# Kernel tuning notes

Hardware: AMD Instinct MI355X
Metric: run time of the kernel (lower is better)

## Reference

```python
import jax, jax.numpy as jnp
import numpy as np

N = 50000      # nodes
E = 800000     # edges (before self-loops)
F_IN = 256     # nfeat
HEADS = 8      # nhead
C1 = 16        # hidden_sizes (per-head channels of conv1)
NCLS = 40      # nclass
NEG_SLOPE = 0.2


def setup_inputs() -> dict:
    key = jax.random.key(0)
    ks = jax.random.split(key, 12)
    s = 0.1
    x = jax.random.normal(ks[0], (N, F_IN), dtype=jnp.float32)
    edge_index = jax.random.randint(ks[1], (2, E), 0, N, dtype=jnp.int64)
    edge_attr = jax.random.normal(ks[2], (E,), dtype=jnp.float32)  # unused by forward
    W1 = jax.random.normal(ks[3], (F_IN, HEADS * C1), dtype=jnp.float32) * s
    att_src1 = jax.random.normal(ks[4], (HEADS, C1), dtype=jnp.float32) * s
    att_dst1 = jax.random.normal(ks[5], (HEADS, C1), dtype=jnp.float32) * s
    b1 = jnp.zeros((HEADS * C1,), dtype=jnp.float32)
    W2 = jax.random.normal(ks[6], (HEADS * C1, NCLS), dtype=jnp.float32) * s
    att_src2 = jax.random.normal(ks[7], (1, NCLS), dtype=jnp.float32) * s
    att_dst2 = jax.random.normal(ks[8], (1, NCLS), dtype=jnp.float32) * s
    b2 = jnp.zeros((NCLS,), dtype=jnp.float32)
    return {"x": x, "edge_index": edge_index, "edge_attr": edge_attr,
            "W1": W1, "att_src1": att_src1, "att_dst1": att_dst1, "b1": b1,
            "W2": W2, "att_src2": att_src2, "att_dst2": att_dst2, "b2": b2}


def gat_layer(x, W, att_src, att_dst, bias, src, dst, concat):
    """PyG-style GATConv (eval mode, no dropout). src/dst include self-loops."""
    H, C = att_src.shape
    h = (x @ W).reshape(-1, H, C)                     # [N,H,C]
    a_src = (h * att_src[None]).sum(-1)               # [N,H]
    a_dst = (h * att_dst[None]).sum(-1)               # [N,H]
    e = jax.nn.leaky_relu(a_src[src] + a_dst[dst], NEG_SLOPE)  # [Etot,H]
    # segment softmax over destination neighborhoods
    m = jax.ops.segment_max(e, dst, num_segments=N)   # [N,H]
    m = jax.lax.stop_gradient(jnp.where(jnp.isfinite(m), m, 0.0))
    p = jnp.exp(e - m[dst])
    denom = jax.ops.segment_sum(p, dst, num_segments=N)
    alpha = p / (denom[dst] + 1e-16)                  # [Etot,H]
    out = jax.ops.segment_sum(alpha[:, :, None] * h[src], dst, num_segments=N)  # [N,H,C]
    out = out.reshape(-1, H * C) if concat else out.mean(axis=1)
    return out + bias


def reference(x, edge_index, edge_attr, W1, att_src1, att_dst1, b1, W2, att_src2, att_dst2, b2):
    # add self loops (PyG GATConv default)
    loops = jnp.arange(N, dtype=edge_index.dtype)
    src = jnp.concatenate([edge_index[0], loops])
    dst = jnp.concatenate([edge_index[1], loops])
    # eval mode: F.dropout is identity
    h = jax.nn.elu(gat_layer(x, W1, att_src1, att_dst1, b1, src, dst, concat=True))
    final = gat_layer(h, W2, att_src2, att_dst2, b2, src, dst, concat=False)
    return final, jax.nn.log_softmax(final, axis=1)
```

## Files before the change

### kernel.cpp

```cpp
#include <hip/hip_runtime.h>

#define NN 50000
#define EE 800000
#define FIN 256
#define HD 8
#define C1 16
#define HC 128
#define NC 40
#define NEG 0.2f
#define CAP 64
#define R2 32
#define BM 64
#define NB_P 98
#define GB1 (NB_P * 8)
#define NP_N (NN / 8)

typedef __attribute__((ext_vector_type(8))) short short8;
typedef __attribute__((ext_vector_type(4))) float f32x4;
union FragU { uint4 u; short8 s; };

__device__ __forceinline__ float leaky(float v){ return v > 0.f ? v : NEG * v; }

__device__ __forceinline__ unsigned int f2bf(float f){
  unsigned int u = __float_as_uint(f);
  u += 0x7fffu + ((u >> 16) & 1u);
  return u >> 16;
}
__device__ __forceinline__ unsigned int pack2bf(float a, float b){
  return f2bf(a) | (f2bf(b) << 16);
}
__device__ __forceinline__ float bflo(unsigned int u){ return __uint_as_float(u << 16); }
__device__ __forceinline__ float bfhi(unsigned int u){ return __uint_as_float(u & 0xffff0000u); }

__global__ __launch_bounds__(256) void k_prep(const float* __restrict__ W1,
                                              uint4* __restrict__ W1bfs){
  int f = blockIdx.x * 256 + threadIdx.x;
  int lane = f & 63, nt = (f >> 6) & 7, kt = f >> 9;
  int quad = lane >> 4, l16 = lane & 15;
  const float* src = W1 + (size_t)(kt * 32 + quad * 8) * HC + nt * 16 + l16;
  unsigned int p[4];
#pragma unroll
  for (int jj = 0; jj < 4; jj++){
    float v0 = src[(size_t)(2 * jj) * HC];
    float v1 = src[(size_t)(2 * jj + 1) * HC];
    p[jj] = pack2bf(v0, v1);
  }
  W1bfs[f] = make_uint4(p[0], p[1], p[2], p[3]);
}

__global__ __launch_bounds__(256) void k_gemm1(const float* __restrict__ x,
                                               const uint4* __restrict__ W1bfs,
                                               const float* __restrict__ att_s,
                                               const float* __restrict__ att_d,
                                               const int* __restrict__ ei,
                                               unsigned short* __restrict__ h1b,
                                               float* __restrict__ as1,
                                               float* __restrict__ ad1,
                                               int* __restrict__ cnt,
                                               int* __restrict__ srcp){
  const int tid = threadIdx.x;
  const int part = blockIdx.x & 7, rank = blockIdx.x >> 3;
  const int lo = part * NP_N, hi = lo + NP_N;
  for (int e = rank * 256 + tid; e < EE; e += NB_P * 256){
    int d = ei[EE + e];
    if (d >= lo && d < hi){
      int s = ei[e];
      int pos = atomicAdd(&cnt[d], 1);
      if (pos < CAP) srcp[d * CAP + pos] = s;
    }
  }

  const int wave = tid >> 6, lane = tid & 63;
  const int quad = lane >> 4, l16 = lane & 15;
  const int m0 = blockIdx.x * BM + wave * 16;
  int arow = m0 + l16; if (arow >= NN) arow = NN - 1;
  const float* xr = x + (size_t)arow * FIN;

  f32x4 acc[8];
#pragma unroll
  for (int t = 0; t < 8; t++) acc[t] = (f32x4){0.f, 0.f, 0.f, 0.f};

#pragma unroll
  for (int kt = 0; kt < 8; kt++){
    const float4 a0 = *(const float4*)(xr + kt * 32 + quad * 8);
    const float4 a1 = *(const float4*)(xr + kt * 32 + quad * 8 + 4);
    FragU af;
    af.u = make_uint4(pack2bf(a0.x, a0.y), pack2bf(a0.z, a0.w),
                      pack2bf(a1.x, a1.y), pack2bf(a1.z, a1.w));
    FragU bf[8];
#pragma unroll
    for (int nt = 0; nt < 8; nt++)
      bf[nt].u = W1bfs[(kt * 8 + nt) * 64 + lane];
#pragma unroll
    for (int nt = 0; nt < 8; nt++)
      acc[nt] = __builtin_amdgcn_mfma_f32_16x16x32_bf16(af.s, bf[nt].s, acc[nt], 0, 0, 0);
  }

  float sv[8], dv[8];
#pragma unroll
  for (int h = 0; h < 8; h++){ sv[h] = att_s[h * 16 + l16]; dv[h] = att_d[h * 16 + l16]; }
#pragma unroll
  for (int r = 0; r < 4; r++){
    const int gr = m0 + quad * 4 + r;
    float s[8], d[8];
#pragma unroll
    for (int h = 0; h < 8; h++){ s[h] = acc[h][r] * sv[h]; d[h] = acc[h][r] * dv[h]; }
#pragma unroll
    for (int o = 1; o < 16; o <<= 1){
#pragma unroll
      for (int h = 0; h < 8; h++){ s[h] += __shfl_xor(s[h], o); d[h] += __shfl_xor(d[h], o); }
    }
    if (gr < NN){
#pragma unroll
      for (int h = 0; h < 8; h++)
        h1b[(size_t)gr * HC + h * 16 + l16] = (unsigned short)f2bf(acc[h][r]);
      if (l16 == 0){
        *(float4*)(as1 + gr * 8)     = make_float4(s[0], s[1], s[2], s[3]);
        *(float4*)(as1 + gr * 8 + 4) = make_float4(s[4], s[5], s[6], s[7]);
        *(float4*)(ad1 + gr * 8)     = make_float4(d[0], d[1], d[2], d[3]);
        *(float4*)(ad1 + gr * 8 + 4) = make_float4(d[4], d[5], d[6], d[7]);
      }
    }
  }
}

__global__ __launch_bounds__(64) void k_agg1(const int* __restrict__ srcp,
                                             const int* __restrict__ cnt,
                                             const float* __restrict__ as1,
                                             const float* __restrict__ ad1,
                                             const unsigned short* __restrict__ h1b,
                                             const float* __restrict__ b1,
                                             unsigned short* __restrict__ h2b){
  const int n = blockIdx.x, lane = threadIdx.x;
  const int q = lane >> 4, t = lane & 15, h = t >> 1;
  const int base = n * CAP;
  int deg = cnt[n]; if (deg > CAP) deg = CAP;
  const float adg = ad1[n * 8 + h];
  float m = -3.0e38f, den = 0.f;
  float acc[8];
#pragma unroll
  for (int c = 0; c < 8; c++) acc[c] = 0.f;

  if (q == 0){
    const uint4 hv = *(const uint4*)(h1b + (size_t)n * HC + t * 8);
    m = leaky(as1[n * 8 + h] + adg);
    den = 1.f;
    acc[0] = bflo(hv.x); acc[1] = bfhi(hv.x);
    acc[2] = bflo(hv.y); acc[3] = bfhi(hv.y);
    acc[4] = bflo(hv.z); acc[5] = bfhi(hv.z);
    acc[6] = bflo(hv.w); acc[7] = bfhi(hv.w);
  }

  int i = q;
  int sA = (i < deg) ? srcp[base + i] : n;
  uint4 hA = *(const uint4*)(h1b + (size_t)sA * HC + t * 8);
  float aA = as1[sA * 8 + h];
  int sB = (i + 4 < deg) ? srcp[base + i + 4] : n;
  while (i < deg){
    const uint4 hB = *(const uint4*)(h1b + (size_t)sB * HC + t * 8);
    const float aB = as1[sB * 8 + h];
    const int sC = (i + 8 < deg) ? srcp[base + i + 8] : n;
    float v = leaky(aA + adg);
    float mn = fmaxf(m, v);
    float r = __expf(m - mn), w = __expf(v - mn);
    den = den * r + w;
    acc[0] = acc[0] * r + w * bflo(hA.x); acc[1] = acc[1] * r + w * bfhi(hA.x);
    acc[2] = acc[2] * r + w * bflo(hA.y); acc[3] = acc[3] * r + w * bfhi(hA.y);
    acc[4] = acc[4] * r + w * bflo(hA.z); acc[5] = acc[5] * r + w * bfhi(hA.z);
    acc[6] = acc[6] * r + w * bflo(hA.w); acc[7] = acc[7] * r + w * bfhi(hA.w);
    m = mn;
    hA = hB; aA = aB; sA = sB; sB = sC;
    i += 4;
  }
#pragma unroll
  for (int o = 16; o <= 32; o <<= 1){
    float mo = __shfl_xor(m, o);
    float dno = __shfl_xor(den, o);
    float mn = fmaxf(m, mo);
    float ra = __expf(m - mn), rb = __expf(mo - mn);
    den = den * ra + dno * rb;
#pragma unroll
    for (int c = 0; c < 8; c++){
      float ao = __shfl_xor(acc[c], o);
      acc[c] = acc[c] * ra + ao * rb;
    }
    m = mn;
  }
  if (q == 0){
    float invd = 1.f / (den + 1e-16f);
    float o8[8];
    const float4 bA = *(const float4*)(b1 + t * 8);
    const float4 bB = *(const float4*)(b1 + t * 8 + 4);
    o8[0] = acc[0] * invd + bA.x; o8[1] = acc[1] * invd + bA.y;
    o8[2] = acc[2] * invd + bA.z; o8[3] = acc[3] * invd + bA.w;
    o8[4] = acc[4] * invd + bB.x; o8[5] = acc[5] * invd + bB.y;
    o8[6] = acc[6] * invd + bB.z; o8[7] = acc[7] * invd + bB.w;
#pragma unroll
    for (int c = 0; c < 8; c++) o8[c] = (o8[c] > 0.f) ? o8[c] : (__expf(o8[c]) - 1.f);
    uint4 pk;
    pk.x = pack2bf(o8[0], o8[1]); pk.y = pack2bf(o8[2], o8[3]);
    pk.z = pack2bf(o8[4], o8[5]); pk.w = pack2bf(o8[6], o8[7]);
    *(uint4*)(h2b + (size_t)n * HC + t * 8) = pk;
  }
}

__global__ __launch_bounds__(256) void k_gemm2(const unsigned short* __restrict__ h2b,
                                               const float* __restrict__ W2,
                                               const float* __restrict__ att_s2,
                                               const float* __restrict__ att_d2,
                                               unsigned short* __restrict__ gb,
                                               float* __restrict__ as2,
                                               float* __restrict__ ad2){
  __shared__ float hs[R2][HC + 2];
  __shared__ float w2s[HC * NC];
  const int tid = threadIdx.x;
  const int r0 = blockIdx.x * R2;
  for (int i = tid; i < HC * NC; i += 256) w2s[i] = W2[i];
  for (int i = tid; i < R2 * (HC / 2); i += 256){
    int r = i / (HC / 2), c = i % (HC / 2);
    unsigned int u = (r0 + r < NN) ? ((const unsigned int*)h2b)[(size_t)(r0 + r) * (HC / 2) + c] : 0u;
    hs[r][2 * c]     = bflo(u);
    hs[r][2 * c + 1] = bfhi(u);
  }
  __syncthreads();
  const int r = tid >> 3, j = tid & 7;
  float acc[5] = {0.f, 0.f, 0.f, 0.f, 0.f};
  for (int k = 0; k < HC; k++){
    float hv = hs[r][k];
#pragma unroll
    for (int q = 0; q < 5; q++) acc[q] += hv * w2s[k * NC + j + 8 * q];
  }
  const int node = r0 + r;
  if (node < NN){
    float s = 0.f, d = 0.f;
#pragma unroll
    for (int q = 0; q < 5; q++){
      int c = j + 8 * q;
      gb[(size_t)node * NC + c] = (unsigned short)f2bf(acc[q]);
      s += acc[q] * att_s2[c];
      d += acc[q] * att_d2[c];
    }
#pragma unroll
    for (int o = 1; o < 8; o <<= 1){ s += __shfl_xor(s, o); d += __shfl_xor(d, o); }
    if (j == 0){ as2[node] = s; ad2[node] = d; }
  }
}

__global__ __launch_bounds__(64) void k_agg2(const int* __restrict__ srcp,
                                             const int* __restrict__ cnt,
                                             const float* __restrict__ as2,
                                             const float* __restrict__ ad2,
                                             const unsigned short* __restrict__ gb,
                                             const float* __restrict__ b2,
                                             float* __restrict__ out){
  const int n = blockIdx.x, lane = threadIdx.x;
  const int half = lane >> 5, c2 = lane & 31;
  const int base = n * CAP;
  int deg = cnt[n]; if (deg > CAP) deg = CAP;
  const float ad = ad2[n];
  const bool act = (c2 < 20);
  float m = -3.0e38f, den = 0.f, ax = 0.f, ay = 0.f;
  if (half == 0){
    m = leaky(as2[n] + ad);
    den = 1.f;
    if (act){
      unsigned int u = *(const unsigned int*)(gb + (size_t)n * NC + c2 * 2);
      ax = bflo(u); ay = bfhi(u);
    }
  }
  int i = half;
  int sA = (i < deg) ? srcp[base + i] : n;
  while (i < deg){
    int sB = (i + 2 < deg) ? srcp[base + i + 2] : n;
    float v = leaky(as2[sA] + ad);
    float gx = 0.f, gy = 0.f;
    if (act){
      unsigned int u = *(const unsigned int*)(gb + (size_t)sA * NC + c2 * 2);
      gx = bflo(u); gy = bfhi(u);
    }
    float mn = fmaxf(m, v);
    float r = __expf(m - mn), w = __expf(v - mn);
    den = den * r + w;
    ax = ax * r + w * gx; ay = ay * r + w * gy;
    m = mn;
    sA = sB; i += 2;
  }
  float mo = __shfl_xor(m, 32), dno = __shfl_xor(den, 32);
  float bx = __shfl_xor(ax, 32), by = __shfl_xor(ay, 32);
  float mn = fmaxf(m, mo);
  float ra = __expf(m - mn), rb = __expf(mo - mn);
  den = den * ra + dno * rb;
  ax = ax * ra + bx * rb; ay = ay * ra + by * rb;
  __shared__ float fin[NC];
  if (half == 0 && act){
    float invd = 1.f / (den + 1e-16f);
    float f0 = ax * invd + b2[c2 * 2];
    float f1 = ay * invd + b2[c2 * 2 + 1];
    out[(size_t)n * NC + c2 * 2]     = f0;
    out[(size_t)n * NC + c2 * 2 + 1] = f1;
    fin[c2 * 2] = f0; fin[c2 * 2 + 1] = f1;
  }
  __syncthreads();
  float v = (lane < NC) ? fin[lane] : -3.4e38f;
  float mx = v;
#pragma unroll
  for (int o = 32; o; o >>= 1) mx = fmaxf(mx, __shfl_xor(mx, o));
  float ex = (lane < NC) ? __expf(v - mx) : 0.f;
#pragma unroll
  for (int o = 32; o; o >>= 1) ex += __shfl_xor(ex, o);
  float lse = mx + __logf(ex);
  if (lane < NC) out[(size_t)(NN * NC) + (size_t)n * NC + lane] = v - lse;
}

extern "C" void kernel_launch(void* const* d_in, const int* in_sizes, int n_in,
                              void* d_out, int out_size, void* d_ws, size_t ws_size,
                              hipStream_t stream){
  const float* x      = (const float*)d_in[0];
  const int*   ei     = (const int*)  d_in[1];
  const float* W1     = (const float*)d_in[3];
  const float* att_s1 = (const float*)d_in[4];
  const float* att_d1 = (const float*)d_in[5];
  const float* b1     = (const float*)d_in[6];
  const float* W2     = (const float*)d_in[7];
  const float* att_s2 = (const float*)d_in[8];
  const float* att_d2 = (const float*)d_in[9];
  const float* b2     = (const float*)d_in[10];
  float* out = (float*)d_out;

  char* wp = (char*)d_ws;
  uint4* W1bfs = (uint4*)wp;                 wp += (size_t)4096 * 16;
  unsigned short* h1b = (unsigned short*)wp; wp += (size_t)NN * HC * 2;
  unsigned short* h2b = (unsigned short*)wp; wp += (size_t)NN * HC * 2;
  unsigned short* gb  = (unsigned short*)wp; wp += (size_t)NN * NC * 2;
  float* as1 = (float*)wp;                   wp += (size_t)NN * HD * 4;
  float* ad1 = (float*)wp;                   wp += (size_t)NN * HD * 4;
  float* as2 = (float*)wp;                   wp += (size_t)NN * 4;
  float* ad2 = (float*)wp;                   wp += (size_t)NN * 4;
  int* cnt   = (int*)wp;                     wp += (size_t)NN * 4;
  int* srcp  = (int*)wp;                     wp += (size_t)NN * CAP * 4;

  hipMemsetAsync(cnt, 0, (size_t)NN * sizeof(int), stream);
  k_prep  <<<16, 256, 0, stream>>>(W1, W1bfs);
  k_gemm1 <<<GB1, 256, 0, stream>>>(x, W1bfs, att_s1, att_d1, ei, h1b, as1, ad1, cnt, srcp);
  k_agg1  <<<NN, 64, 0, stream>>>(srcp, cnt, as1, ad1, h1b, b1, h2b);
  k_gemm2 <<<(NN + R2 - 1) / R2, 256, 0, stream>>>(h2b, W2, att_s2, att_d2, gb, as2, ad2);
  k_agg2  <<<NN, 64, 0, stream>>>(srcp, cnt, as2, ad2, gb, b2, out);
}
```

Measured before the change: 289.2 us.

## Pre-bin edges by destination partition before adjacency build in GEMM1

```diff
diff --git a/kernel.cpp b/kernel.cpp
--- a/kernel.cpp
+++ b/kernel.cpp
@@ -14,6 +14,10 @@
 #define NB_P 98
 #define GB1 (NB_P * 8)
 #define NP_N (NN / 8)
+#define PCAP 150000
+#define BIN_CH 1024
+#define BIN_B ((EE + BIN_CH - 1) / BIN_CH)
+#define SCAP 256
 
 typedef __attribute__((ext_vector_type(8))) short short8;
 typedef __attribute__((ext_vector_type(4))) float f32x4;
@@ -48,11 +52,54 @@
   W1bfs[f] = make_uint4(p[0], p[1], p[2], p[3]);
 }
 
+__global__ __launch_bounds__(256) void k_bin(const int* __restrict__ ei,
+                                             uint2* __restrict__ pairs,
+                                             int* __restrict__ gcur){
+  __shared__ int lcnt[8];
+  __shared__ int gbase[8];
+  __shared__ uint2 stage[8 * SCAP];
+  const int tid = threadIdx.x;
+  if (tid < 8) lcnt[tid] = 0;
+  __syncthreads();
+  const int e0 = blockIdx.x * BIN_CH;
+#pragma unroll
+  for (int j = 0; j < 4; j++){
+    int e = e0 + tid + 256 * j;
+    if (e < EE){
+      int s = ei[e], d = ei[EE + e];
+      int p = d / NP_N;
+      int pos = atomicAdd(&lcnt[p], 1);
+      if (pos < SCAP) stage[p * SCAP + pos] = make_uint2((unsigned)d, (unsigned)s);
+    }
+  }
+  __syncthreads();
+  if (tid < 8){
+    int c = lcnt[tid]; if (c > SCAP) c = SCAP;
+    gbase[tid] = atomicAdd(&gcur[tid], c);
+  }
+  __syncthreads();
+  int pfx[9]; pfx[0] = 0;
+#pragma unroll
+  for (int p = 0; p < 8; p++){
+    int c = lcnt[p]; if (c > SCAP) c = SCAP;
+    pfx[p + 1] = pfx[p] + c;
+  }
+  const int total = pfx[8];
+  for (int i = tid; i < total; i += 256){
+    int p = 0;
+    while (i >= pfx[p + 1]) p++;
+    int k = i - pfx[p];
+    size_t dst = (size_t)p * PCAP + gbase[p] + k;
+    if (gbase[p] + k < PCAP) pairs[dst] = stage[p * SCAP + k];
+  }
+}
+
 __global__ __launch_bounds__(256) void k_gemm1(const float* __restrict__ x,
                                                const uint4* __restrict__ W1bfs,
                                                const float* __restrict__ att_s,
                                                const float* __restrict__ att_d,
-                                               const int* __restrict__ ei,
+                                               const uint2* __restrict__ pairs,
+                                               const int* __restrict__ gcur,
                                                unsigned short* __restrict__ h1b,
                                                float* __restrict__ as1,
                                                float* __restrict__ ad1,
@@ -60,14 +107,13 @@
                                                int* __restrict__ srcp){
   const int tid = threadIdx.x;
   const int part = blockIdx.x & 7, rank = blockIdx.x >> 3;
-  const int lo = part * NP_N, hi = lo + NP_N;
-  for (int e = rank * 256 + tid; e < EE; e += NB_P * 256){
-    int d = ei[EE + e];
-    if (d >= lo && d < hi){
-      int s = ei[e];
-      int pos = atomicAdd(&cnt[d], 1);
-      if (pos < CAP) srcp[d * CAP + pos] = s;
-    }
+  int tot = gcur[part]; if (tot > PCAP) tot = PCAP;
+  const uint2* pp = pairs + (size_t)part * PCAP;
+  for (int i = rank * 256 + tid; i < tot; i += NB_P * 256){
+    uint2 pr = pp[i];
+    int d = (int)pr.x, s = (int)pr.y;
+    int pos = atomicAdd(&cnt[d], 1);
+    if (pos < CAP) srcp[d * CAP + pos] = s;
   }
 
   const int wave = tid >> 6, lane = tid & 63;
@@ -329,6 +375,7 @@
 
   char* wp = (char*)d_ws;
   uint4* W1bfs = (uint4*)wp;                 wp += (size_t)4096 * 16;
+  uint2* pairs = (uint2*)wp;                 wp += (size_t)8 * PCAP * 8;
   unsigned short* h1b = (unsigned short*)wp; wp += (size_t)NN * HC * 2;
   unsigned short* h2b = (unsigned short*)wp; wp += (size_t)NN * HC * 2;
   unsigned short* gb  = (unsigned short*)wp; wp += (size_t)NN * NC * 2;
@@ -337,11 +384,14 @@
   float* as2 = (float*)wp;                   wp += (size_t)NN * 4;
   float* ad2 = (float*)wp;                   wp += (size_t)NN * 4;
   int* cnt   = (int*)wp;                     wp += (size_t)NN * 4;
+  int* gcur  = (int*)wp;                     wp += (size_t)32;
   int* srcp  = (int*)wp;                     wp += (size_t)NN * CAP * 4;
 
-  hipMemsetAsync(cnt, 0, (size_t)NN * sizeof(int), stream);
+  hipMemsetAsync(cnt, 0, (size_t)NN * sizeof(int) + 32, stream);
   k_prep  <<<16, 256, 0, stream>>>(W1, W1bfs);
-  k_gemm1 <<<GB1, 256, 0, stream>>>(x, W1bfs, att_s1, att_d1, ei, h1b, as1, ad1, cnt, srcp);
+  k_bin   <<<BIN_B, 256, 0, stream>>>(ei, pairs, gcur);
+  k_gemm1 <<<GB1, 256, 0, stream>>>(x, W1bfs, att_s1, att_d1, pairs, gcur,
+                                    h1b, as1, ad1, cnt, srcp);
   k_agg1  <<<NN, 64, 0, stream>>>(srcp, cnt, as1, ad1, h1b, b1, h2b);
   k_gemm2 <<<(NN + R2 - 1) / R2, 256, 0, stream>>>(h2b, W2, att_s2, att_d2, gb, as2, ad2);
   k_agg2  <<<NN, 64, 0, stream>>>(srcp, cnt, as2, ad2, gb, b2, out);
```

Measured after the change: 300.9 us. +4.0%, slower.
